# Kernel tuning notes

Hardware: AMD Instinct MI355X
Metric: run time of the kernel (lower is better)

The kernel has to match this reference:

```python
import jax, jax.numpy as jnp
import numpy as np

B, IN_C, CH = 16384, 128, 512
EMBED_DIM = 6240          # = 64*64 + 64 + 64*32 + 32 (BatchDecoder param count)
NUM_EMB = 512
DEC_IN, DEC_H, DATA_Y = 64, 64, 32


def setup_inputs() -> dict:
    key = jax.random.key(0)
    ks = jax.random.split(key, 16)
    s = lambda fan_in: 1.0 / np.sqrt(fan_in)
    return {
        "x":   jax.random.normal(ks[0], (B, IN_C), jnp.float32),
        # enc_f: Linear(IN_C,CH) -> ReLU -> Linear(CH,EMBED_DIM)
        "Wf1": jax.random.normal(ks[1], (IN_C, CH), jnp.float32) * s(IN_C),
        "bf1": jax.random.normal(ks[2], (CH,), jnp.float32) * s(IN_C),
        "Wf2": jax.random.normal(ks[3], (CH, EMBED_DIM), jnp.float32) * s(CH),
        "bf2": jax.random.normal(ks[4], (EMBED_DIM,), jnp.float32) * s(CH),
        # enc_x: Linear(IN_C,CH) -> ReLU -> Linear(CH,DEC_IN)
        "Wx1": jax.random.normal(ks[5], (IN_C, CH), jnp.float32) * s(IN_C),
        "bx1": jax.random.normal(ks[6], (CH,), jnp.float32) * s(IN_C),
        "Wx2": jax.random.normal(ks[7], (CH, DEC_IN), jnp.float32) * s(CH),
        "bx2": jax.random.normal(ks[8], (DEC_IN,), jnp.float32) * s(CH),
        # VQ codebook: [dim, num_embeddings] as in Quantize
        "embed": jax.random.normal(ks[9], (EMBED_DIM, NUM_EMB), jnp.float32),
        # BatchDecoder per-codeword MLP parameters (nets' own init params;
        # the original's weight-injection loop is a no-op: `p = new_vec` only
        # rebinds a local, so the nets run with their initialized weights)
        "W1": jax.random.normal(ks[10], (NUM_EMB, DEC_IN, DEC_H), jnp.float32) * s(DEC_IN),
        "b1": jax.random.normal(ks[11], (NUM_EMB, DEC_H), jnp.float32) * s(DEC_IN),
        "W2": jax.random.normal(ks[12], (NUM_EMB, DEC_H, DATA_Y), jnp.float32) * s(DEC_H),
        "b2": jax.random.normal(ks[13], (NUM_EMB, DATA_Y), jnp.float32) * s(DEC_H),
    }


def reference(x, Wf1, bf1, Wf2, bf2, Wx1, bx1, Wx2, bx2, embed, W1, b1, W2, b2):
    # ---- encode: enc_f MLP -> [B, EMBED_DIM] ----
    pre_f = jax.nn.relu(x @ Wf1 + bf1) @ Wf2 + bf2
    # ---- Quantize (eval mode; EMA buffer updates are side effects only) ----
    # dist[b,k] = ||pre_f[b]||^2 - 2 pre_f[b].embed[:,k] + ||embed[:,k]||^2
    dist = (jnp.sum(pre_f * pre_f, axis=1, keepdims=True)
            - 2.0 * (pre_f @ embed)
            + jnp.sum(embed * embed, axis=0, keepdims=True))  # [B, K]
    embed_ind = jnp.argmin(dist, axis=1)                       # [B]
    encodings = jax.nn.one_hot(embed_ind, NUM_EMB, dtype=pre_f.dtype)
    quantize = embed.T[embed_ind]                              # [B, EMBED_DIM]
    diff = jnp.mean((jax.lax.stop_gradient(quantize) - pre_f) ** 2)
    z_q = pre_f + jax.lax.stop_gradient(quantize - pre_f)      # straight-through (unused by buggy decoder)
    avg_probs = jnp.mean(encodings, axis=0)
    perplexity = jnp.exp(-jnp.sum(avg_probs * jnp.log(avg_probs + 1e-10)))
    # ---- enc_x MLP -> [B, DEC_IN] ----
    embedded_x = jax.nn.relu(x @ Wx1 + bx1) @ Wx2 + bx2
    # ---- BatchDecoder: per-sample expert MLP dispatch by embed_ind ----
    h = jax.nn.relu(jnp.einsum('bi,bih->bh', embedded_x, W1[embed_ind]) + b1[embed_ind])
    dec = jnp.einsum('bh,bho->bo', h, W2[embed_ind]) + b2[embed_ind]  # [B, DATA_Y]
    return (dec, diff, embed_ind, perplexity)
```

## Files before the change

kernel.cpp:

```cpp
#include <hip/hip_runtime.h>
#include <math.h>

#define BN     16384
#define INC    128
#define CH     512
#define ED     6240
#define KN     512
#define DIN    64
#define DH     64
#define DY     32
#define NCW    195
#define CHP    (CH + 8)

#define OUT_DEC   0
#define OUT_DIFF  (BN*DY)
#define OUT_IND   (BN*DY + 1)
#define OUT_PERP  (BN*DY + 1 + BN)

typedef _Float16 half8 __attribute__((ext_vector_type(8)));
typedef float    f32x4 __attribute__((ext_vector_type(4)));
#define MFMA16(a, b, c) __builtin_amdgcn_mfma_f32_16x16x32_f16(a, b, c, 0, 0, 0)

__device__ __forceinline__ size_t paddr(int tile, int NC, int c, int lane, int e) {
    return ((size_t)(tile * NC + c) * 64 + lane) * 8 + e;
}

__global__ __launch_bounds__(256) void packall_kernel(
        const float* __restrict__ x,
        const float* __restrict__ Wf1, const float* __restrict__ Wx1,
        const float* __restrict__ bf1, const float* __restrict__ bx1,
        const float* __restrict__ Wx2,
        const float* __restrict__ Wf2, const float* __restrict__ bf2,
        const float* __restrict__ embed,
        _Float16* __restrict__ XPs, _Float16* __restrict__ XPl,
        _Float16* __restrict__ WfxPs, _Float16* __restrict__ WfxPl,
        float* __restrict__ bfx,
        _Float16* __restrict__ Wx2Ps, _Float16* __restrict__ Wx2Pl,
        _Float16* __restrict__ WfPs, _Float16* __restrict__ WfPl,
        _Float16* __restrict__ EmPs, _Float16* __restrict__ EmPl,
        float* __restrict__ s2p, float* __restrict__ bep,
        float* __restrict__ w0) {
    __shared__ __align__(16) char smem[16384];
    int id = blockIdx.x;
    int t = threadIdx.x;
    if (id < 12480) {
        float (*red)[33] = (float(*)[33])smem;
        int bx = id % NCW, by = id / NCW;
        int d = bx * 32 + (t & 31);
        int j = by * 8 + (t >> 5);
        float v = Wf2[(size_t)j * ED + d];
        _Float16 hi = (_Float16)v;
        size_t a = paddr(j >> 4, NCW, d >> 5, ((d & 31) >> 3) * 16 + (j & 15), d & 7);
        WfPs[a] = hi;
        WfPl[a] = (_Float16)(v - (float)hi);
        red[t >> 5][t & 31] = v * bf2[d];
        __syncthreads();
        if (t < 8) {
            float s = 0.f;
            #pragma unroll
            for (int i = 0; i < 32; ++i) s += red[t][i];
            atomicAdd(&w0[by * 8 + t], s);
        }
    } else if (id < 15600) {
        float (*tile)[33] = (float(*)[33])smem;
        int sub = id - 12480;
        int bx = sub % NCW, by = sub / NCW;
        int dl = t >> 5, kl = t & 31;
        #pragma unroll
        for (int r = 0; r < 4; ++r)
            tile[dl + 8 * r][kl] = embed[(size_t)(bx * 32 + dl + 8 * r) * KN
                                         + by * 32 + kl];
        __syncthreads();
        int d = bx * 32 + kl;
        #pragma unroll
        for (int r = 0; r < 4; ++r) {
            int k = by * 32 + dl + 8 * r;
            float v = tile[kl][dl + 8 * r];
            _Float16 hi = (_Float16)v;
            size_t a = paddr(k >> 4, NCW, d >> 5, ((d & 31) >> 3) * 16 + (k & 15), d & 7);
            EmPs[a] = hi;
            EmPl[a] = (_Float16)(v - (float)hi);
        }
    } else if (id < 15728) {
        float (*rs)[33] = (float(*)[33])smem;
        float (*rb)[33] = (float(*)[33])(smem + 8 * 33 * 4);
        int sub = id - 15600;
        int bx = sub % 16, by = sub / 16;
        int kl = t & 31, dl = t >> 5;
        int kb = bx * 32;
        int d0 = by * 780;
        float s = 0.f, b = 0.f;
        for (int d = d0 + dl; d < d0 + 780; d += 8) {
            float e = embed[(size_t)d * KN + kb + kl];
            s = fmaf(e, e, s);
            b = fmaf(bf2[d], e, b);
        }
        rs[dl][kl] = s; rb[dl][kl] = b;
        __syncthreads();
        if (t < 32) {
            float ss = 0.f, bb = 0.f;
            #pragma unroll
            for (int i = 0; i < 8; ++i) { ss += rs[i][t]; bb += rb[i][t]; }
            s2p[by * KN + kb + t] = ss;
            bep[by * KN + kb + t] = bb;
        }
    } else if (id < 16240) {
        float (*xt)[INC] = (float(*)[INC])smem;
        int m0 = (id - 15728) * 32;
        for (int i = t; i < 32 * (INC / 4); i += 256) {
            int row = i >> 5, c4 = (i & 31) << 2;
            *(float4*)&xt[row][c4] = *(const float4*)&x[(size_t)(m0 + row) * INC + c4];
        }
        __syncthreads();
        int ta = m0 >> 4;
        #pragma unroll
        for (int i = 0; i < 2; ++i) {
            int idx = t + 256 * i;
            int tile2 = idx >> 8;
            int c = (idx >> 6) & 3;
            int lane = idx & 63;
            int m = tile2 * 16 + (lane & 15);
            int d0 = c * 32 + ((lane >> 4) << 3);
            half8 hh, ll;
            #pragma unroll
            for (int e = 0; e < 8; ++e) {
                float v = xt[m][d0 + e];
                _Float16 hi = (_Float16)v;
                hh[e] = hi;
                ll[e] = (_Float16)(v - (float)hi);
            }
            *(half8*)(XPs + paddr(ta + tile2, 4, c, lane, 0)) = hh;
            *(half8*)(XPl + paddr(ta + tile2, 4, c, lane, 0)) = ll;
        }
    } else if (id < 16304) {
        int tile = id - 16240;
        for (int i = t; i < 2048; i += 256) {
            int c = i >> 9, lane = (i >> 3) & 63, e = i & 7;
            int n = tile * 16 + (lane & 15);
            int d = c * 32 + ((lane >> 4) << 3) + e;
            float v = (n < 512) ? Wf1[(size_t)d * CH + n] : Wx1[(size_t)d * CH + n - 512];
            _Float16 hi = (_Float16)v;
            size_t a = paddr(tile, 4, c, lane, e);
            WfxPs[a] = hi;
            WfxPl[a] = (_Float16)(v - (float)hi);
        }
        if (tile == 0)
            for (int j = t; j < 512; j += 256) { bfx[j] = bf1[j]; bfx[512 + j] = bx1[j]; }
    } else {
        int tile = id - 16304;
        for (int i = t; i < 8192; i += 256) {
            int c = i >> 9, lane = (i >> 3) & 63, e = i & 7;
            int n = tile * 16 + (lane & 15);
            int d = c * 32 + ((lane >> 4) << 3) + e;
            float v = Wx2[(size_t)d * DIN + n];
            _Float16 hi = (_Float16)v;
            size_t a = paddr(tile, 16, c, lane, e);
            Wx2Ps[a] = hi;
            Wx2Pl[a] = (_Float16)(v - (float)hi);
        }
    }
}

__global__ __launch_bounds__(512) void mfma_weg_kernel(
        const _Float16* __restrict__ WfPs, const _Float16* __restrict__ WfPl,
        const _Float16* __restrict__ EmPs, const _Float16* __restrict__ EmPl,
        float* __restrict__ WeP, float* __restrict__ GP) {
    int t = threadIdx.x;
    int w = t >> 6, L = t & 63;
    int lane16 = L & 15, quad = L >> 4;
    int m0 = blockIdx.x * 128 + (w & 3) * 32;
    int n0 = blockIdx.y * 128 + (w >> 2) * 64;
    int ta = m0 >> 4, tb = n0 >> 4;
    int zraw = blockIdx.z;
    bool isWe = zraw < 8;
    int z = isWe ? zraw : zraw - 8;
    int base = NCW / 8, rem = NCW % 8;
    int c0 = z * base + (z < rem ? z : rem);
    int cnt = base + (z < rem ? 1 : 0);
    f32x4 acc[2][4];
    #pragma unroll
    for (int rt = 0; rt < 2; ++rt)
        #pragma unroll
        for (int tt = 0; tt < 4; ++tt) acc[rt][tt] = (f32x4){0.f, 0.f, 0.f, 0.f};
    if (isWe) {
        for (int ci = 0; ci < cnt; ++ci) {
            int c = c0 + ci;
            size_t oa0 = paddr(ta, NCW, c, L, 0), oa1 = paddr(ta + 1, NCW, c, L, 0);
            half8 A0h = *(const half8*)(WfPs + oa0);
            half8 A0l = *(const half8*)(WfPl + oa0);
            half8 A1h = *(const half8*)(WfPs + oa1);
            half8 A1l = *(const half8*)(WfPl + oa1);
            #pragma unroll
            for (int tt = 0; tt < 4; ++tt) {
                size_t ob = paddr(tb + tt, NCW, c, L, 0);
                half8 Bh = *(const half8*)(EmPs + ob);
                half8 Bl8 = *(const half8*)(EmPl + ob);
                acc[0][tt] = MFMA16(A0h, Bl8, MFMA16(A0l, Bh, MFMA16(A0h, Bh, acc[0][tt])));
                acc[1][tt] = MFMA16(A1h, Bl8, MFMA16(A1l, Bh, MFMA16(A1h, Bh, acc[1][tt])));
            }
        }
    } else {
        for (int ci = 0; ci < cnt; ++ci) {
            int c = c0 + ci;
            half8 A0h = *(const half8*)(WfPs + paddr(ta, NCW, c, L, 0));
            half8 A1h = *(const half8*)(WfPs + paddr(ta + 1, NCW, c, L, 0));
            #pragma unroll
            for (int tt = 0; tt < 4; ++tt) {
                half8 Bh = *(const half8*)(WfPs + paddr(tb + tt, NCW, c, L, 0));
                acc[0][tt] = MFMA16(A0h, Bh, acc[0][tt]);
                acc[1][tt] = MFMA16(A1h, Bh, acc[1][tt]);
            }
        }
    }
    float* C = (isWe ? WeP : GP) + (size_t)z * KN * KN;
    #pragma unroll
    for (int rt = 0; rt < 2; ++rt)
        #pragma unroll
        for (int tt = 0; tt < 4; ++tt)
            #pragma unroll
            for (int r = 0; r < 4; ++r)
                C[(size_t)(m0 + rt * 16 + quad * 4 + r) * KN
                  + n0 + tt * 16 + lane16] = acc[rt][tt][r];
}

__global__ __launch_bounds__(256) void wepackgred_kernel(
        const float* __restrict__ WeP, const float* __restrict__ GP,
        const float* __restrict__ s2p, const float* __restrict__ bep,
        _Float16* __restrict__ WePs, _Float16* __restrict__ WePl,
        float* __restrict__ G, float* __restrict__ s2, float* __restrict__ be) {
    int id = blockIdx.x;
    int t = threadIdx.x;
    if (id < 1024) {
        int g = id * 256 + t;
        int j = g >> 9, k = g & 511;
        float v = 0.f;
        #pragma unroll
        for (int z = 0; z < 8; ++z) v += WeP[(size_t)z * KN * KN + g];
        _Float16 hi = (_Float16)v;
        size_t a = paddr(k >> 4, 16, j >> 5, ((j & 31) >> 3) * 16 + (k & 15), j & 7);
        WePs[a] = hi;
        WePl[a] = (_Float16)(v - (float)hi);
    } else if (id < 2048) {
        int g = (id - 1024) * 256 + t;
        float v = 0.f;
        #pragma unroll
        for (int z = 0; z < 8; ++z) v += GP[(size_t)z * KN * KN + g];
        G[g] = v;
    } else {
        #pragma unroll
        for (int i = 0; i < 2; ++i) {
            int k = t + 256 * i;
            float s = 0.f, b = 0.f;
            #pragma unroll
            for (int y = 0; y < 8; ++y) {
                s += s2p[y * KN + k];
                b += bep[y * KN + k];
            }
            s2[k] = s;
            be[k] = b;
        }
    }
}

__global__ __launch_bounds__(512) void enc1_kernel(
        const _Float16* __restrict__ XPs, const _Float16* __restrict__ XPl,
        const _Float16* __restrict__ WfxPs, const _Float16* __restrict__ WfxPl,
        const float* __restrict__ bfx,
        const _Float16* __restrict__ Wx2Ps, const _Float16* __restrict__ Wx2Pl,
        const float* __restrict__ bx2,
        const _Float16* __restrict__ WePs, const _Float16* __restrict__ WePl,
        const float* __restrict__ s2, const float* __restrict__ be,
        _Float16* __restrict__ HTP, float* __restrict__ colsum,
        float* __restrict__ EX,
        int* __restrict__ ind, float* __restrict__ out_ind,
        int* __restrict__ counts, float* __restrict__ diffsum) {
    __shared__ _Float16 hhi[32][CHP];
    __shared__ _Float16 hlo[32][CHP];
    __shared__ float redv[8][32];
    __shared__ int   redi[8][32];
    __shared__ float fin[32];
    int t = threadIdx.x;
    int w = t >> 6, L = t & 63;
    int l16 = L & 15, quad = L >> 4;
    int m0 = blockIdx.x * 32;
    int ta = m0 >> 4;
    int enc = blockIdx.y;
    int n0 = enc * 512 + w * 64;
    int tb = n0 >> 4;
    f32x4 acc[2][4];
    #pragma unroll
    for (int rt = 0; rt < 2; ++rt)
        #pragma unroll
        for (int tt = 0; tt < 4; ++tt) acc[rt][tt] = (f32x4){0.f, 0.f, 0.f, 0.f};
    #pragma unroll
    for (int c = 0; c < 4; ++c) {
        size_t oa0 = paddr(ta, 4, c, L, 0), oa1 = paddr(ta + 1, 4, c, L, 0);
        half8 A0h = *(const half8*)(XPs + oa0);
        half8 A0l = *(const half8*)(XPl + oa0);
        half8 A1h = *(const half8*)(XPs + oa1);
        half8 A1l = *(const half8*)(XPl + oa1);
        #pragma unroll
        for (int tt = 0; tt < 4; ++tt) {
            size_t ob = paddr(tb + tt, 4, c, L, 0);
            half8 Bh = *(const half8*)(WfxPs + ob);
            half8 Bl8 = *(const half8*)(WfxPl + ob);
            acc[0][tt] = MFMA16(A0h, Bl8, MFMA16(A0l, Bh, MFMA16(A0h, Bh, acc[0][tt])));
            acc[1][tt] = MFMA16(A1h, Bl8, MFMA16(A1l, Bh, MFMA16(A1h, Bh, acc[1][tt])));
        }
    }
    #pragma unroll
    for (int rt = 0; rt < 2; ++rt)
        #pragma unroll
        for (int tt = 0; tt < 4; ++tt) {
            int col = w * 64 + tt * 16 + l16;
            float bias = bfx[enc * 512 + col];
            #pragma unroll
            for (int r = 0; r < 4; ++r) {
                int row = rt * 16 + quad * 4 + r;
                float v = fmaxf(acc[rt][tt][r] + bias, 0.f);
                _Float16 hi = (_Float16)v;
                hhi[row][col] = hi;
                hlo[row][col] = (_Float16)(v - (float)hi);
            }
        }
    __syncthreads();
    if (enc == 0) {
        float s = 0.f;
        #pragma unroll
        for (int r = 0; r < 32; ++r) s += (float)hhi[r][t] + (float)hlo[r][t];
        atomicAdd(&colsum[t], s);
        int cb = blockIdx.x;
        #pragma unroll
        for (int i = 0; i < 4; ++i) {
            int idx = t + 512 * i;
            int chtile = idx >> 6;
            int lane = idx & 63;
            int ch = chtile * 16 + (lane & 15);
            int b0 = (lane >> 4) << 3;
            half8 hh;
            #pragma unroll
            for (int e = 0; e < 8; ++e) hh[e] = hhi[b0 + e][ch];
            *(half8*)(HTP + paddr(chtile, 512, cb, lane, 0)) = hh;
        }
        int colbase = w * 64;
        int tbs = w * 4;
        float cks[4];
        #pragma unroll
        for (int tt = 0; tt < 4; ++tt) {
            int c = colbase + tt * 16 + l16;
            cks[tt] = 0.5f * s2[c] - be[c];
        }
        #pragma unroll
        for (int rt = 0; rt < 2; ++rt)
            #pragma unroll
            for (int tt = 0; tt < 4; ++tt) acc[rt][tt] = (f32x4){0.f, 0.f, 0.f, 0.f};
        for (int c = 0; c < 16; ++c) {
            int d0 = c * 32 + (quad << 3);
            int mA0 = l16, mA1 = 16 + l16;
            half8 A0h = *(const half8*)(&hhi[mA0][d0]);
            half8 A0l = *(const half8*)(&hlo[mA0][d0]);
            half8 A1h = *(const half8*)(&hhi[mA1][d0]);
            half8 A1l = *(const half8*)(&hlo[mA1][d0]);
            #pragma unroll
            for (int tt = 0; tt < 4; ++tt) {
                size_t ob = paddr(tbs + tt, 16, c, L, 0);
                half8 Bh = *(const half8*)(WePs + ob);
                half8 Bl8 = *(const half8*)(WePl + ob);
                acc[0][tt] = MFMA16(A0h, Bl8, MFMA16(A0l, Bh, MFMA16(A0h, Bh, acc[0][tt])));
                acc[1][tt] = MFMA16(A1h, Bl8, MFMA16(A1l, Bh, MFMA16(A1h, Bh, acc[1][tt])));
            }
        }
        #pragma unroll
        for (int rt = 0; rt < 2; ++rt) {
            #pragma unroll
            for (int r = 0; r < 4; ++r) {
                float mv = cks[0] - acc[rt][0][r];
                int mi = colbase + l16;
                #pragma unroll
                for (int tt = 1; tt < 4; ++tt) {
                    float v = cks[tt] - acc[rt][tt][r];
                    int c = colbase + tt * 16 + l16;
                    if (v < mv || (v == mv && c < mi)) { mv = v; mi = c; }
                }
                #pragma unroll
                for (int d = 1; d < 16; d <<= 1) {
                    float ov = __shfl_xor(mv, d);
                    int oi = __shfl_xor(mi, d);
                    if (ov < mv || (ov == mv && oi < mi)) { mv = ov; mi = oi; }
                }
                if (l16 == 0) {
                    int row = rt * 16 + quad * 4 + r;
                    redv[w][row] = mv; redi[w][row] = mi;
                }
            }
        }
        __syncthreads();
        if (t < 32) {
            float mv = redv[0][t]; int mi = redi[0][t];
            #pragma unroll
            for (int w2 = 1; w2 < 8; ++w2) {
                float ov = redv[w2][t]; int oi = redi[w2][t];
                if (ov < mv || (ov == mv && oi < mi)) { mv = ov; mi = oi; }
            }
            int b = m0 + t;
            ind[b] = mi;
            out_ind[b] = (float)mi;
            atomicAdd(&counts[mi], 1);
            fin[t] = 2.f * mv;
        }
        __syncthreads();
        if (t == 0) {
            float s = 0.f;
            #pragma unroll
            for (int i = 0; i < 32; ++i) s += fin[i];
            atomicAdd(diffsum, s);
        }
    } else {
        int rt = w & 1, ct = w >> 1;
        f32x4 eacc = (f32x4){0.f, 0.f, 0.f, 0.f};
        for (int c = 0; c < 16; ++c) {
            int d0 = c * 32 + (quad << 3);
            int m = rt * 16 + l16;
            half8 Ah = *(half8*)(&hhi[m][d0]);
            half8 Al = *(half8*)(&hlo[m][d0]);
            size_t ob = paddr(ct, 16, c, L, 0);
            half8 Bh = *(const half8*)(Wx2Ps + ob);
            half8 Bl8 = *(const half8*)(Wx2Pl + ob);
            eacc = MFMA16(Ah, Bl8, MFMA16(Al, Bh, MFMA16(Ah, Bh, eacc)));
        }
        int col = ct * 16 + l16;
        float bias = bx2[col];
        #pragma unroll
        for (int r = 0; r < 4; ++r) {
            int row = m0 + rt * 16 + quad * 4 + r;
            EX[(size_t)row * DIN + col] = eacc[r] + bias;
        }
    }
}

__global__ __launch_bounds__(512) void hth_kernel(const _Float16* __restrict__ HTP,
                                                  const float* __restrict__ G,
                                                  float* __restrict__ diffsum) {
    __shared__ float sf[512];
    int t = threadIdx.x;
    int w = t >> 6, L = t & 63;
    int lane16 = L & 15, quad = L >> 4;
    int m0 = blockIdx.x * 128 + (w & 3) * 32;
    int n0 = blockIdx.y * 128 + (w >> 2) * 64;
    int ta = m0 >> 4, tb = n0 >> 4;
    int c0 = blockIdx.z * 16;
    f32x4 acc[2][4];
    #pragma unroll
    for (int rt = 0; rt < 2; ++rt)
        #pragma unroll
        for (int tt = 0; tt < 4; ++tt) acc[rt][tt] = (f32x4){0.f, 0.f, 0.f, 0.f};
    for (int ci = 0; ci < 16; ++ci) {
        int c = c0 + ci;
        half8 A0h = *(const half8*)(HTP + paddr(ta, 512, c, L, 0));
        half8 A1h = *(const half8*)(HTP + paddr(ta + 1, 512, c, L, 0));
        #pragma unroll
        for (int tt = 0; tt < 4; ++tt) {
            half8 Bh = *(const half8*)(HTP + paddr(tb + tt, 512, c, L, 0));
            acc[0][tt] = MFMA16(A0h, Bh, acc[0][tt]);
            acc[1][tt] = MFMA16(A1h, Bh, acc[1][tt]);
        }
    }
    float s = 0.f;
    #pragma unroll
    for (int rt = 0; rt < 2; ++rt)
        #pragma unroll
        for (int tt = 0; tt < 4; ++tt)
            #pragma unroll
            for (int r = 0; r < 4; ++r)
                s += acc[rt][tt][r] * G[(size_t)(m0 + rt * 16 + quad * 4 + r) * KN
                                        + n0 + tt * 16 + lane16];
    sf[t] = s;
    __syncthreads();
    for (int st = 256; st > 0; st >>= 1) {
        if (t < st) sf[t] += sf[t + st];
        __syncthreads();
    }
    if (t == 0) atomicAdd(diffsum, sf[0]);
}

__global__ __launch_bounds__(512) void finalize_kernel(const int* __restrict__ counts,
                                                       const float* __restrict__ diffsum,
                                                       const float* __restrict__ colsum,
                                                       const float* __restrict__ w0,
                                                       const float* __restrict__ bf2,
                                                       float* __restrict__ out_diff,
                                                       float* __restrict__ out_perp) {
    __shared__ float sf[512];
    int t = threadIdx.x;
    int c = counts[t];
    double p = (double)c / (double)BN;
    double term = -p * log(p + 1e-10);
    float dotp = colsum[t] * w0[t];
    float bbp = 0.f;
    for (int d = t; d < ED; d += 512) { float v = bf2[d]; bbp = fmaf(v, v, bbp); }
    sf[t] = dotp; __syncthreads();
    for (int s = 256; s > 0; s >>= 1) { if (t < s) sf[t] += sf[t + s]; __syncthreads(); }
    float dot_all = sf[0];
    __syncthreads();
    sf[t] = bbp; __syncthreads();
    for (int s = 256; s > 0; s >>= 1) { if (t < s) sf[t] += sf[t + s]; __syncthreads(); }
    float bb = sf[0];
    __syncthreads();
    sf[t] = (float)term; __syncthreads();
    for (int s = 256; s > 0; s >>= 1) { if (t < s) sf[t] += sf[t + s]; __syncthreads(); }
    if (t == 0) {
        *out_perp = expf(sf[0]);
        *out_diff = (diffsum[0] + 2.f * dot_all + (float)BN * bb) /
                    ((float)BN * (float)ED);
    }
}

__global__ __launch_bounds__(256) void scatter_kernel(const int* __restrict__ ind,
                                                      const int* __restrict__ counts,
                                                      int* __restrict__ cursors,
                                                      int* __restrict__ perm) {
    __shared__ int sc[KN], soff[KN], lcount[KN], lbase[KN], lcur[KN];
    int t = threadIdx.x;
    for (int i = t; i < KN; i += 256) {
        sc[i] = counts[i];
        lcount[i] = 0; lcur[i] = 0;
    }
    __syncthreads();
    #pragma unroll
    for (int half = 0; half < 2; ++half) {
        int i = t + 256 * half;
        int off = 0;
        for (int k = 0; k < i; ++k) off += sc[k];
        soff[i] = off;
    }
    int b = blockIdx.x * 256 + t;
    int k = ind[b];
    atomicAdd(&lcount[k], 1);
    __syncthreads();
    for (int i = t; i < KN; i += 256) {
        int c = lcount[i];
        if (c > 0) lbase[i] = atomicAdd(&cursors[i], c);
    }
    __syncthreads();
    int pos = soff[k] + lbase[k] + atomicAdd(&lcur[k], 1);
    perm[pos] = b;
}

__global__ __launch_bounds__(256) void decode_kernel(const float* __restrict__ EX,
                                                     const int* __restrict__ perm,
                                                     const int* __restrict__ ind,
                                                     const float* __restrict__ W1,
                                                     const float* __restrict__ b1,
                                                     const float* __restrict__ W2,
                                                     const float* __restrict__ b2,
                                                     float* __restrict__ dec) {
    __shared__ float exs[4][DIN];
    __shared__ float h2s[4][DH];
    int t = threadIdx.x;
    int w = t >> 6, l = t & 63;
    int s = blockIdx.x * 4 + w;
    int b = perm[s];
    int k = ind[b];
    exs[w][l] = EX[(size_t)b * DIN + l];
    __syncthreads();
    const float* w1 = W1 + (size_t)k * (DIN * DH);
    float h = b1[(size_t)k * DH + l];
    #pragma unroll
    for (int j = 0; j < DIN; ++j)
        h = fmaf(exs[w][j], w1[(size_t)j * DH + l], h);
    h2s[w][l] = fmaxf(h, 0.f);
    __syncthreads();
    if (l < DY) {
        const float* w2 = W2 + (size_t)k * (DH * DY);
        float d = b2[(size_t)k * DY + l];
        #pragma unroll
        for (int j = 0; j < DH; ++j)
            d = fmaf(h2s[w][j], w2[(size_t)j * DY + l], d);
        dec[(size_t)b * DY + l] = d;
    }
}

extern "C" void kernel_launch(void* const* d_in, const int* in_sizes, int n_in,
                              void* d_out, int out_size, void* d_ws, size_t ws_size,
                              hipStream_t stream) {
    const float* x     = (const float*)d_in[0];
    const float* Wf1   = (const float*)d_in[1];
    const float* bf1   = (const float*)d_in[2];
    const float* Wf2   = (const float*)d_in[3];
    const float* bf2   = (const float*)d_in[4];
    const float* Wx1   = (const float*)d_in[5];
    const float* bx1   = (const float*)d_in[6];
    const float* Wx2   = (const float*)d_in[7];
    const float* bx2   = (const float*)d_in[8];
    const float* embed = (const float*)d_in[9];
    const float* W1    = (const float*)d_in[10];
    const float* b1    = (const float*)d_in[11];
    const float* W2    = (const float*)d_in[12];
    const float* b2    = (const float*)d_in[13];
    float* out = (float*)d_out;

    char* ws = (char*)d_ws;
    size_t off = 0;
    auto carve = [&](size_t bytes) -> void* {
        void* p = ws + off;
        off += (bytes + 255) & ~(size_t)255;
        return p;
    };
    _Float16* XPs   = (_Float16*)carve((size_t)BN * INC * 2);
    _Float16* XPl   = (_Float16*)carve((size_t)BN * INC * 2);
    _Float16* WfxPs = (_Float16*)carve((size_t)1024 * INC * 2);
    _Float16* WfxPl = (_Float16*)carve((size_t)1024 * INC * 2);
    float*    bfx   = (float*)carve(1024 * 4);
    _Float16* Wx2Ps = (_Float16*)carve((size_t)DIN * CH * 2);
    _Float16* Wx2Pl = (_Float16*)carve((size_t)DIN * CH * 2);
    _Float16* WfPs  = (_Float16*)carve((size_t)CH * ED * 2);
    _Float16* WfPl  = (_Float16*)carve((size_t)CH * ED * 2);
    _Float16* EmPs  = (_Float16*)carve((size_t)KN * ED * 2);
    _Float16* EmPl  = (_Float16*)carve((size_t)KN * ED * 2);
    char* un = (char*)carve((size_t)BN * CH * 2);
    float*    WeP = (float*)un;
    float*    GP  = (float*)(un + (size_t)8 * KN * KN * 4);
    _Float16* HTP = (_Float16*)un;
    _Float16* WePs = (_Float16*)carve((size_t)KN * CH * 2);
    _Float16* WePl = (_Float16*)carve((size_t)KN * CH * 2);
    float*    G    = (float*)carve((size_t)KN * KN * 4);
    float*    EX   = (float*)carve((size_t)BN * DIN * 4);
    float*    s2p  = (float*)carve(8 * KN * 4);
    float*    bep  = (float*)carve(8 * KN * 4);
    float*    s2   = (float*)carve(KN * 4);
    float*    be   = (float*)carve(KN * 4);
    char* zbase = ws + off;
    float* w0    = (float*)carve(CH * 4);
    float* colsum= (float*)carve(CH * 4);
    int*   counts= (int*)carve(KN * 4);
    int*   cursors=(int*)carve(KN * 4);
    float* diffsum=(float*)carve(256);
    size_t zbytes = (size_t)(ws + off - zbase);
    int*   ind     = (int*)carve(BN * 4);
    int*   perm    = (int*)carve(BN * 4);
    (void)in_sizes; (void)n_in; (void)out_size; (void)ws_size;

    hipMemsetAsync(zbase, 0, zbytes, stream);
    packall_kernel<<<16308, 256, 0, stream>>>(x, Wf1, Wx1, bf1, bx1, Wx2, Wf2, bf2,
                                              embed, XPs, XPl, WfxPs, WfxPl, bfx,
                                              Wx2Ps, Wx2Pl, WfPs, WfPl, EmPs, EmPl,
                                              s2p, bep, w0);
    mfma_weg_kernel<<<dim3(4, 4, 16), 512, 0, stream>>>(WfPs, WfPl, EmPs, EmPl,
                                                        WeP, GP);
    wepackgred_kernel<<<2049, 256, 0, stream>>>(WeP, GP, s2p, bep,
                                                WePs, WePl, G, s2, be);
    enc1_kernel<<<dim3(BN / 32, 2), 512, 0, stream>>>(XPs, XPl, WfxPs, WfxPl, bfx,
                                                      Wx2Ps, Wx2Pl, bx2,
                                                      WePs, WePl, s2, be,
                                                      HTP, colsum, EX,
                                                      ind, out + OUT_IND, counts,
                                                      diffsum);
    scatter_kernel<<<BN / 256, 256, 0, stream>>>(ind, counts, cursors, perm);
    decode_kernel<<<BN / 4, 256, 0, stream>>>(EX, perm, ind, W1, b1, W2, b2,
                                              out + OUT_DEC);
    hth_kernel<<<dim3(4, 4, 32), 512, 0, stream>>>(HTP, G, diffsum);
    finalize_kernel<<<1, 512, 0, stream>>>(counts, diffsum, colsum, w0, bf2,
                                           out + OUT_DIFF, out + OUT_PERP);
}
```

Measured before the change: 356.0 us.

## Fuse H^T H · G trace term into enc1 via per-tile quadratic form

Replaces the separate hth kernel, which formed the 512x512 H^T H Gram matrix over all samples and dotted it with G, with a per-block computation inside enc1. Each block now computes H·G on its own 32 rows using a packed fp16 G and takes the row-wise dot with H. This removes the HTP transposed store and its later reload, plus one launch. In exchange the MFMA work grows from a single H^T H pass to a per-row H·G pass, and G is kept only in single fp16 rather than hi/lo, which risks precision loss in diff.

```diff
diff --git a/kernel.cpp b/kernel.cpp
--- a/kernel.cpp
+++ b/kernel.cpp
@@ -227,7 +227,8 @@
         const float* __restrict__ WeP, const float* __restrict__ GP,
         const float* __restrict__ s2p, const float* __restrict__ bep,
         _Float16* __restrict__ WePs, _Float16* __restrict__ WePl,
-        float* __restrict__ G, float* __restrict__ s2, float* __restrict__ be) {
+        _Float16* __restrict__ GhPs, float* __restrict__ s2,
+        float* __restrict__ be) {
     int id = blockIdx.x;
     int t = threadIdx.x;
     if (id < 1024) {
@@ -242,10 +243,12 @@
         WePl[a] = (_Float16)(v - (float)hi);
     } else if (id < 2048) {
         int g = (id - 1024) * 256 + t;
+        int m = g >> 9, n = g & 511;
         float v = 0.f;
         #pragma unroll
         for (int z = 0; z < 8; ++z) v += GP[(size_t)z * KN * KN + g];
-        G[g] = v;
+        GhPs[paddr(n >> 4, 16, m >> 5, ((m & 31) >> 3) * 16 + (n & 15), m & 7)]
+            = (_Float16)v;
     } else {
         #pragma unroll
         for (int i = 0; i < 2; ++i) {
@@ -269,8 +272,9 @@
         const _Float16* __restrict__ Wx2Ps, const _Float16* __restrict__ Wx2Pl,
         const float* __restrict__ bx2,
         const _Float16* __restrict__ WePs, const _Float16* __restrict__ WePl,
+        const _Float16* __restrict__ GhPs,
         const float* __restrict__ s2, const float* __restrict__ be,
-        _Float16* __restrict__ HTP, float* __restrict__ colsum,
+        float* __restrict__ colsum,
         float* __restrict__ EX,
         int* __restrict__ ind, float* __restrict__ out_ind,
         int* __restrict__ counts, float* __restrict__ diffsum) {
@@ -279,6 +283,7 @@
     __shared__ float redv[8][32];
     __shared__ int   redi[8][32];
     __shared__ float fin[32];
+    __shared__ float gpart[8];
     int t = threadIdx.x;
     int w = t >> 6, L = t & 63;
     int l16 = L & 15, quad = L >> 4;
@@ -329,19 +334,6 @@
         #pragma unroll
         for (int r = 0; r < 32; ++r) s += (float)hhi[r][t] + (float)hlo[r][t];
         atomicAdd(&colsum[t], s);
-        int cb = blockIdx.x;
-        #pragma unroll
-        for (int i = 0; i < 4; ++i) {
-            int idx = t + 512 * i;
-            int chtile = idx >> 6;
-            int lane = idx & 63;
-            int ch = chtile * 16 + (lane & 15);
-            int b0 = (lane >> 4) << 3;
-            half8 hh;
-            #pragma unroll
-            for (int e = 0; e < 8; ++e) hh[e] = hhi[b0 + e][ch];
-            *(half8*)(HTP + paddr(chtile, 512, cb, lane, 0)) = hh;
-        }
         int colbase = w * 64;
         int tbs = w * 4;
         float cks[4];
@@ -394,6 +386,36 @@
                 }
             }
         }
+        #pragma unroll
+        for (int rt = 0; rt < 2; ++rt)
+            #pragma unroll
+            for (int tt = 0; tt < 4; ++tt) acc[rt][tt] = (f32x4){0.f, 0.f, 0.f, 0.f};
+        for (int c = 0; c < 16; ++c) {
+            int d0 = c * 32 + (quad << 3);
+            half8 A0h = *(const half8*)(&hhi[l16][d0]);
+            half8 A1h = *(const half8*)(&hhi[16 + l16][d0]);
+            #pragma unroll
+            for (int tt = 0; tt < 4; ++tt) {
+                half8 Bh = *(const half8*)(GhPs + paddr(tbs + tt, 16, c, L, 0));
+                acc[0][tt] = MFMA16(A0h, Bh, acc[0][tt]);
+                acc[1][tt] = MFMA16(A1h, Bh, acc[1][tt]);
+            }
+        }
+        float gs = 0.f;
+        #pragma unroll
+        for (int rt = 0; rt < 2; ++rt)
+            #pragma unroll
+            for (int tt = 0; tt < 4; ++tt) {
+                int col = colbase + tt * 16 + l16;
+                #pragma unroll
+                for (int r = 0; r < 4; ++r) {
+                    int row = rt * 16 + quad * 4 + r;
+                    gs += acc[rt][tt][r] * (float)hhi[row][col];
+                }
+            }
+        #pragma unroll
+        for (int d = 1; d < 64; d <<= 1) gs += __shfl_xor(gs, d);
+        if (L == 0) gpart[w] = gs;
         __syncthreads();
         if (t < 32) {
             float mv = redv[0][t]; int mi = redi[0][t];
@@ -413,6 +435,8 @@
             float s = 0.f;
             #pragma unroll
             for (int i = 0; i < 32; ++i) s += fin[i];
+            #pragma unroll
+            for (int w2 = 0; w2 < 8; ++w2) s += gpart[w2];
             atomicAdd(diffsum, s);
         }
     } else {
@@ -436,51 +460,6 @@
             EX[(size_t)row * DIN + col] = eacc[r] + bias;
         }
     }
-}
-
-__global__ __launch_bounds__(512) void hth_kernel(const _Float16* __restrict__ HTP,
-                                                  const float* __restrict__ G,
-                                                  float* __restrict__ diffsum) {
-    __shared__ float sf[512];
-    int t = threadIdx.x;
-    int w = t >> 6, L = t & 63;
-    int lane16 = L & 15, quad = L >> 4;
-    int m0 = blockIdx.x * 128 + (w & 3) * 32;
-    int n0 = blockIdx.y * 128 + (w >> 2) * 64;
-    int ta = m0 >> 4, tb = n0 >> 4;
-    int c0 = blockIdx.z * 16;
-    f32x4 acc[2][4];
-    #pragma unroll
-    for (int rt = 0; rt < 2; ++rt)
-        #pragma unroll
-        for (int tt = 0; tt < 4; ++tt) acc[rt][tt] = (f32x4){0.f, 0.f, 0.f, 0.f};
-    for (int ci = 0; ci < 16; ++ci) {
-        int c = c0 + ci;
-        half8 A0h = *(const half8*)(HTP + paddr(ta, 512, c, L, 0));
-        half8 A1h = *(const half8*)(HTP + paddr(ta + 1, 512, c, L, 0));
-        #pragma unroll
-        for (int tt = 0; tt < 4; ++tt) {
-            half8 Bh = *(const half8*)(HTP + paddr(tb + tt, 512, c, L, 0));
-            acc[0][tt] = MFMA16(A0h, Bh, acc[0][tt]);
-            acc[1][tt] = MFMA16(A1h, Bh, acc[1][tt]);
-        }
-    }
-    float s = 0.f;
-    #pragma unroll
-    for (int rt = 0; rt < 2; ++rt)
-        #pragma unroll
-        for (int tt = 0; tt < 4; ++tt)
-            #pragma unroll
-            for (int r = 0; r < 4; ++r)
-                s += acc[rt][tt][r] * G[(size_t)(m0 + rt * 16 + quad * 4 + r) * KN
-                                        + n0 + tt * 16 + lane16];
-    sf[t] = s;
-    __syncthreads();
-    for (int st = 256; st > 0; st >>= 1) {
-        if (t < st) sf[t] += sf[t + st];
-        __syncthreads();
-    }
-    if (t == 0) atomicAdd(diffsum, sf[0]);
 }
 
 __global__ __launch_bounds__(512) void finalize_kernel(const int* __restrict__ counts,
@@ -620,10 +599,9 @@
     char* un = (char*)carve((size_t)BN * CH * 2);
     float*    WeP = (float*)un;
     float*    GP  = (float*)(un + (size_t)8 * KN * KN * 4);
-    _Float16* HTP = (_Float16*)un;
     _Float16* WePs = (_Float16*)carve((size_t)KN * CH * 2);
     _Float16* WePl = (_Float16*)carve((size_t)KN * CH * 2);
-    float*    G    = (float*)carve((size_t)KN * KN * 4);
+    _Float16* GhPs = (_Float16*)carve((size_t)KN * KN * 2);
     float*    EX   = (float*)carve((size_t)BN * DIN * 4);
     float*    s2p  = (float*)carve(8 * KN * 4);
     float*    bep  = (float*)carve(8 * KN * 4);
@@ -648,17 +626,16 @@
     mfma_weg_kernel<<<dim3(4, 4, 16), 512, 0, stream>>>(WfPs, WfPl, EmPs, EmPl,
                                                         WeP, GP);
     wepackgred_kernel<<<2049, 256, 0, stream>>>(WeP, GP, s2p, bep,
-                                                WePs, WePl, G, s2, be);
+                                                WePs, WePl, GhPs, s2, be);
     enc1_kernel<<<dim3(BN / 32, 2), 512, 0, stream>>>(XPs, XPl, WfxPs, WfxPl, bfx,
                                                       Wx2Ps, Wx2Pl, bx2,
-                                                      WePs, WePl, s2, be,
-                                                      HTP, colsum, EX,
+                                                      WePs, WePl, GhPs, s2, be,
+                                                      colsum, EX,
                                                       ind, out + OUT_IND, counts,
                                                       diffsum);
     scatter_kernel<<<BN / 256, 256, 0, stream>>>(ind, counts, cursors, perm);
     decode_kernel<<<BN / 4, 256, 0, stream>>>(EX, perm, ind, W1, b1, W2, b2,
                                               out + OUT_DEC);
-    hth_kernel<<<dim3(4, 4, 32), 512, 0, stream>>>(HTP, G, diffsum);
     finalize_kernel<<<1, 512, 0, stream>>>(counts, diffsum, colsum, w0, bf2,
                                            out + OUT_DIFF, out + OUT_PERP);
 }
```

After: 339.7 us. 1.05x faster.
